# Kernel tuning notes

Measured on AMD Instinct MI355X. Metric: run time of the kernel, lower is better.

Reference implementation:

```python
import jax, jax.numpy as jnp
import numpy as np

EPS = 1e-7  # keras.backend.epsilon()
ROUTINGS = 3
NUM_CAPSULE = 32
DIM_CAPSULE = 64


def squash(x, axis=-1):
    # NOTE: faithful to the repo's (non-standard) squash: x / sqrt(||x||^2 + eps)
    s = jnp.sum(jnp.square(x), axis=axis, keepdims=True)
    return x / jnp.sqrt(s + EPS)


def setup_inputs() -> dict:
    key = jax.random.key(0)
    k1, k2 = jax.random.split(key)
    B, N_in, D_in = 64, 1024, 512
    u_vecs = jax.random.normal(k1, (B, N_in, D_in), dtype=jnp.float32)
    # shared capsule kernel: (1, input_dim, num_capsule * dim_capsule)
    W = jax.random.normal(k2, (1, D_in, NUM_CAPSULE * DIM_CAPSULE), dtype=jnp.float32) * (1.0 / np.sqrt(D_in))
    return {"u_vecs": u_vecs, "W": W}


def reference(u_vecs, W):
    B, N_in, D_in = u_vecs.shape
    # K.conv1d with a width-1 kernel == pointwise matmul
    u_hat = jnp.einsum('bid,dz->biz', u_vecs, W[0])  # [B, N_in, NC*DC]
    u_hat = u_hat.reshape(B, N_in, NUM_CAPSULE, DIM_CAPSULE)
    u_hat = jnp.transpose(u_hat, (0, 2, 1, 3))  # [B, NC, N_in, DC]

    b = jnp.zeros((B, NUM_CAPSULE, N_in), dtype=u_hat.dtype)
    outputs = None
    for i in range(ROUTINGS):
        # original permutes b to [B, N_in, NC] and softmaxes the last axis,
        # i.e. softmax over the output-capsule axis (axis=1 here)
        c = jax.nn.softmax(b, axis=1)  # [B, NC, N_in]
        outputs = squash(jnp.einsum('bni,bnid->bnd', c, u_hat))  # [B, NC, DC]
        if i < ROUTINGS - 1:
            b = jnp.einsum('bnd,bnid->bni', outputs, u_hat)  # agreement logits
    return outputs
```

## Files before the change

kernel.cpp:

```cpp
#include <hip/hip_runtime.h>

#define B_SZ   64
#define N_IN   1024
#define D_IN   512
#define NC     32
#define DC     64

typedef unsigned short u16;
typedef unsigned int   u32;
typedef __bf16 bf16x8 __attribute__((ext_vector_type(8)));
typedef _Float16 f16x8 __attribute__((ext_vector_type(8)));
typedef unsigned short u16x8 __attribute__((ext_vector_type(8)));
typedef float f32x4  __attribute__((ext_vector_type(4)));
typedef float f32x16 __attribute__((ext_vector_type(16)));

__device__ __forceinline__ float bf2f(u16 u) {
    unsigned x = ((unsigned)u) << 16;
    return __builtin_bit_cast(float, x);
}
__device__ __forceinline__ u16 f2bf(float f) {
    unsigned x = __builtin_bit_cast(unsigned, f);
    unsigned r = (x + 0x7fffu + ((x >> 16) & 1u)) >> 16;
    return (u16)r;
}
__device__ __forceinline__ u16 f2h(float f) {
    return __builtin_bit_cast(u16, (_Float16)f);
}
__device__ __forceinline__ float h2f(u16 h) {
    return (float)__builtin_bit_cast(_Float16, h);
}

#define ASYNC_LDS16(g, l) __builtin_amdgcn_global_load_lds( \
    (const __attribute__((address_space(1))) void*)(g),     \
    (__attribute__((address_space(3))) void*)(l), 16, 0, 0)

__global__ __launch_bounds__(256) void conv_all(const float* __restrict__ A,
                                                const float* __restrict__ W,
                                                u16* __restrict__ Ab,
                                                u16* __restrict__ Wb,
                                                float* __restrict__ Arowp) {
    const int tid = threadIdx.x;
    if (blockIdx.x >= 1024) {
        const int wb = blockIdx.x - 1024;
#pragma unroll
        for (int it = 0; it < 16; ++it) {
            int i = wb * 4096 + it * 256 + tid;
            float4 v = ((const float4*)W)[i];
            uint2 pk;
            pk.x = (u32)f2bf(v.x) | ((u32)f2bf(v.y) << 16);
            pk.y = (u32)f2bf(v.z) | ((u32)f2bf(v.w) << 16);
            ((uint2*)Wb)[i] = pk;
        }
        return;
    }
    const int b  = blockIdx.x >> 4;
    const int r0 = (blockIdx.x & 15) << 6;
    const int q  = tid & 127;
    const int rh = tid >> 7;
    const size_t rowbase = (size_t)(b * N_IN + r0);
    float a0 = 0.f, a1 = 0.f, a2 = 0.f, a3 = 0.f;
    for (int r = rh; r < 64; r += 2) {
        float4 v = *(const float4*)(A + (rowbase + r) * 512 + q * 4);
        a0 += v.x; a1 += v.y; a2 += v.z; a3 += v.w;
        uint2 pk;
        pk.x = (u32)f2bf(v.x) | ((u32)f2bf(v.y) << 16);
        pk.y = (u32)f2bf(v.z) | ((u32)f2bf(v.w) << 16);
        *(uint2*)(Ab + (rowbase + r) * 512 + q * 4) = pk;
    }
    const int slot = (blockIdx.x & 15) * 2 + rh;
    float* ar = Arowp + ((size_t)b * 32 + slot) * 512 + q * 4;
    ar[0] = a0; ar[1] = a1; ar[2] = a2; ar[3] = a3;
}

__global__ __launch_bounds__(256) void s0_squash(const float* __restrict__ Arowp,
                                                 const u16* __restrict__ Wb,
                                                 float* __restrict__ outs) {
    __shared__ float Al[2 * 512];
    const int tid = threadIdx.x;
    const int z   = blockIdx.x * 256 + tid;
    const int bg  = blockIdx.y * 2;

    for (int t = tid; t < 1024; t += 256) {
        int bb = t >> 9, k = t & 511;
        const float* p = Arowp + ((size_t)(bg + bb) * 32) * 512 + k;
        float s = 0.f;
#pragma unroll
        for (int j = 0; j < 32; ++j) s += p[(size_t)j * 512];
        Al[t] = s;
    }
    __syncthreads();

    float acc[2] = {};
    for (int k = 0; k < 512; ++k) {
        float wv = bf2f(Wb[(size_t)k * 2048 + z]);
        acc[0] += Al[k] * wv;
        acc[1] += Al[512 + k] * wv;
    }
#pragma unroll
    for (int bb = 0; bb < 2; ++bb) {
        float v = acc[bb] * 0.03125f;
        float sq = v * v;
        for (int off = 32; off; off >>= 1) sq += __shfl_xor(sq, off);
        outs[(size_t)(bg + bb) * 2048 + z] = v * (1.0f / sqrtf(sq + 1e-7f));
    }
}

__global__ __launch_bounds__(256) void g_pack(const u16* __restrict__ Wb,
                                              const float* __restrict__ outs,
                                              u16* __restrict__ Gpack) {
    __shared__ float vl[64 * 132];
    const int tid = threadIdx.x;
    const int kt  = blockIdx.x;
    const int np  = blockIdx.y;

    for (int t = tid; t < 8192; t += 256) {
        int b = t >> 7, idx = t & 127;
        vl[b * 132 + idx] = outs[(size_t)b * 2048 + np * 128 + idx];
    }
    __syncthreads();

    const int bs = tid & 15;
    const int k  = kt * 16 + (tid >> 4);
    float acc[4][2] = {};
#pragma unroll
    for (int n2 = 0; n2 < 2; ++n2) {
        const u16* wr = Wb + (size_t)k * 2048 + (np * 2 + n2) * 64;
#pragma unroll
        for (int d8 = 0; d8 < 8; ++d8) {
            u16x8 w8 = *(const u16x8*)&wr[d8 * 8];
            float wf[8];
#pragma unroll
            for (int j = 0; j < 8; ++j) wf[j] = bf2f(w8[j]);
#pragma unroll
            for (int bb = 0; bb < 4; ++bb) {
                const float* vp = &vl[(bs + 16 * bb) * 132 + n2 * 64 + d8 * 8];
                f32x4 va = *(const f32x4*)vp;
                f32x4 vb = *(const f32x4*)(vp + 4);
#pragma unroll
                for (int j = 0; j < 4; ++j) {
                    acc[bb][n2] += wf[j]     * va[j];
                    acc[bb][n2] += wf[j + 4] * vb[j];
                }
            }
        }
    }
    const int kk = k >> 5, kq = k & 31;
#pragma unroll
    for (int bb = 0; bb < 4; ++bb)
#pragma unroll
        for (int n2 = 0; n2 < 2; ++n2) {
            int b = bs + 16 * bb, n = np * 2 + n2;
            Gpack[(((size_t)b * 16 + kk) * 32 + n) * 32 + kq] = f2bf(acc[bb][n2]);
        }
}

__global__ __launch_bounds__(256, 2) void routing_mfma(const u16* __restrict__ Ab,
                                                       const u16* __restrict__ Gpack,
                                                       u16* __restrict__ Mp) {
    __shared__ u16 Al[64 * 512];
    __shared__ u16 clb[64 * 34];
    const int tid   = threadIdx.x;
    const int lane  = tid & 63;
    const int w     = __builtin_amdgcn_readfirstlane(tid >> 6);
    const int b     = blockIdx.x >> 4;
    const int chunk = blockIdx.x & 15;
    const int row0  = chunk * 64;

    const size_t rowbase = (size_t)(b * N_IN + row0);
#pragma unroll
    for (int rr = 0; rr < 16; ++rr) {
        const int r   = w * 16 + rr;
        const int sig = (lane & 56) | ((lane & 7) ^ (r & 7));
        ASYNC_LDS16(Ab + (rowbase + r) * 512 + sig * 8, &Al[r * 512]);
    }
    __syncthreads();

    const int quad = lane >> 4;
    const int l16  = lane & 15;
    f32x4 lacc[2] = {};
    const u16* gb = Gpack + (size_t)b * 16384;
    {
        const int r  = w * 16 + l16;
        const u16* ar = &Al[r * 512];
        for (int kk = 0; kk < 16; ++kk) {
            const int c  = kk * 4 + quad;
            const int cs = (c & 56) | ((c & 7) ^ (r & 7));
            bf16x8 af = *(const bf16x8*)&ar[cs * 8];
#pragma unroll
            for (int nt = 0; nt < 2; ++nt) {
                bf16x8 bf = *(const bf16x8*)&gb[(kk * 32 + nt * 16 + l16) * 32 + quad * 8];
                lacc[nt] = __builtin_amdgcn_mfma_f32_16x16x32_bf16(af, bf, lacc[nt], 0, 0, 0);
            }
        }
    }

#pragma unroll
    for (int reg = 0; reg < 4; ++reg) {
        float m = fmaxf(lacc[0][reg], lacc[1][reg]);
        m = fmaxf(m, __shfl_xor(m, 1));
        m = fmaxf(m, __shfl_xor(m, 2));
        m = fmaxf(m, __shfl_xor(m, 4));
        m = fmaxf(m, __shfl_xor(m, 8));
        float e0 = __expf(lacc[0][reg] - m);
        float e1 = __expf(lacc[1][reg] - m);
        float s = e0 + e1;
        s += __shfl_xor(s, 1);
        s += __shfl_xor(s, 2);
        s += __shfl_xor(s, 4);
        s += __shfl_xor(s, 8);
        float inv = 1.f / s;
        const int row = w * 16 + quad * 4 + reg;
        clb[row * 34 + l16]      = f2bf(e0 * inv);
        clb[row * 34 + 16 + l16] = f2bf(e1 * inv);
    }
    __syncthreads();

    const int h   = lane >> 5;
    const int l32 = lane & 31;
    bf16x8 cfrag[4];
#pragma unroll
    for (int kk2 = 0; kk2 < 4; ++kk2) {
        u16x8 t;
#pragma unroll
        for (int j = 0; j < 8; ++j)
            t[j] = clb[(kk2 * 16 + h * 8 + j) * 34 + l32];
        cfrag[kk2] = __builtin_bit_cast(bf16x8, t);
    }
    u16* mpb = Mp + ((size_t)b * 16 + chunk) * 32 * 512;
    for (int cti = 0; cti < 4; ++cti) {
        const int ct   = w * 4 + cti;
        const int kcol = ct * 32 + l32;
        const int c2   = kcol >> 3;
        const int e    = kcol & 7;
        f32x16 acc = {};
#pragma unroll
        for (int kk2 = 0; kk2 < 4; ++kk2) {
            u16x8 t;
#pragma unroll
            for (int j = 0; j < 8; ++j) {
                const int r2  = kk2 * 16 + h * 8 + j;
                const int cs2 = (c2 & 56) | ((c2 & 7) ^ (r2 & 7));
                t[j] = Al[r2 * 512 + cs2 * 8 + e];
            }
            bf16x8 bf = __builtin_bit_cast(bf16x8, t);
            acc = __builtin_amdgcn_mfma_f32_32x32x16_bf16(cfrag[kk2], bf, acc, 0, 0, 0);
        }
#pragma unroll
        for (int reg = 0; reg < 16; ++reg) {
            const int n = (reg & 3) + 8 * (reg >> 2) + 4 * h;
            mpb[(size_t)n * 512 + kcol] = f2h(acc[reg]);
        }
    }
}

__global__ __launch_bounds__(256, 1) void s_final_mfma(const u16* __restrict__ Mp,
                                                       const u16* __restrict__ Wb,
                                                       float* __restrict__ outs,
                                                       float* __restrict__ outf) {
    __shared__ __align__(16) u16 Wf[32768];
    __shared__ __align__(16) u16 Mlh[16 * 512];
    __shared__ float Sout[8][64];
    const int tid = threadIdx.x;
    const int n   = blockIdx.x;
    const int bg  = blockIdx.y * 8;

    for (int t = tid; t < 8192; t += 256) {
        int k = t >> 4, d4 = t & 15;
        uint2 raw = *(const uint2*)(Wb + (size_t)k * 2048 + n * 64 + d4 * 4);
        u16 bfv[4] = { (u16)(raw.x & 0xffffu), (u16)(raw.x >> 16),
                       (u16)(raw.y & 0xffffu), (u16)(raw.y >> 16) };
        const int kk = k >> 5, quad = (k >> 3) & 3, j = k & 7;
#pragma unroll
        for (int m = 0; m < 4; ++m) {
            int d = d4 * 4 + m, dtile = d >> 4, col = d & 15;
            Wf[(((dtile * 16 + kk) * 4 + quad) * 16 + col) * 8 + j] = f2h(bf2f(bfv[m]));
        }
    }
    for (int t = tid; t < 2048; t += 256) {
        int bs = t >> 8, kp = t & 255;
        const u32* p = (const u32*)(Mp + (((size_t)(bg + bs) * 16) * 32 + n) * 512) + kp;
        float s0 = 0.f, s1 = 0.f;
#pragma unroll
        for (int ch = 0; ch < 16; ++ch) {
            u32 v = p[(size_t)ch * 32 * 256];
            s0 += h2f((u16)(v & 0xffffu));
            s1 += h2f((u16)(v >> 16));
        }
        u32 pk = (u32)f2h(s0) | ((u32)f2h(s1) << 16);
        ((u32*)Mlh)[(bs * 256 + kp) ^ ((bs & 7) << 2)] = pk;
    }
    for (int t = tid; t < 2048; t += 256) ((u32*)Mlh)[2048 + t] = 0;
    __syncthreads();

    const int lane = tid & 63;
    const int w    = tid >> 6;
    const int quad = lane >> 4, l16 = lane & 15;
    f32x4 acc = {};
    for (int kk = 0; kk < 16; ++kk) {
        const int abyte = (l16 * 1024 + kk * 64 + quad * 16) ^ ((l16 & 7) << 4);
        u16x8 a = *(const u16x8*)((const char*)Mlh + abyte);
        u16x8 bfr = *(const u16x8*)&Wf[(((w * 16 + kk) * 4 + quad) * 16 + l16) * 8];
        acc = __builtin_amdgcn_mfma_f32_16x16x32_f16(__builtin_bit_cast(f16x8, a),
                                                     __builtin_bit_cast(f16x8, bfr),
                                                     acc, 0, 0, 0);
    }
    if (quad < 2) {
#pragma unroll
        for (int reg = 0; reg < 4; ++reg)
            Sout[quad * 4 + reg][w * 16 + l16] = acc[reg];
    }
    __syncthreads();

    const int w2 = tid >> 6, d = tid & 63;
#pragma unroll
    for (int i = 0; i < 2; ++i) {
        const int row = w2 * 2 + i, b = bg + row;
        float v = Sout[row][d];
        float sq = v * v;
        for (int off = 32; off; off >>= 1) sq += __shfl_xor(sq, off);
        float o = v * (1.0f / sqrtf(sq + 1e-7f));
        size_t idx = (size_t)b * 2048 + n * 64 + d;
        outs[idx] = o;
        if (outf) outf[idx] = o;
    }
}

extern "C" void kernel_launch(void* const* d_in, const int* in_sizes, int n_in,
                              void* d_out, int out_size, void* d_ws, size_t ws_size,
                              hipStream_t stream) {
    (void)in_sizes; (void)n_in; (void)out_size; (void)ws_size;
    const float* A = (const float*)d_in[0];
    const float* W = (const float*)d_in[1];
    float* out     = (float*)d_out;

    uint8_t* ws = (uint8_t*)d_ws;
    const size_t AB_B    = (size_t)B_SZ * N_IN * D_IN * 2;
    const size_t AROWP_B = (size_t)B_SZ * 32 * D_IN * 4;
    const size_t OUTS_B  = (size_t)B_SZ * NC * DC * 4;
    const size_t GP_B    = (size_t)B_SZ * 16 * 32 * 32 * 2;
    const size_t WB_B    = (size_t)D_IN * NC * DC * 2;
    u16*   Ab    = (u16*)ws;
    float* Arowp = (float*)(ws + AB_B);
    float* outs  = (float*)(ws + AB_B + AROWP_B);
    u16*   Gpack = (u16*)(ws + AB_B + AROWP_B + OUTS_B);
    u16*   Wb    = (u16*)(ws + AB_B + AROWP_B + OUTS_B + GP_B);
    u16*   Mp    = (u16*)(ws + AB_B + AROWP_B + OUTS_B + GP_B + WB_B);

    conv_all<<<1088, 256, 0, stream>>>(A, W, Ab, Wb, Arowp);

    s0_squash<<<dim3(8, 32), 256, 0, stream>>>(Arowp, Wb, outs);

    for (int it = 0; it < 2; ++it) {
        g_pack<<<dim3(32, 16), 256, 0, stream>>>(Wb, outs, Gpack);
        routing_mfma<<<1024, 256, 0, stream>>>(Ab, Gpack, Mp);
        s_final_mfma<<<dim3(32, 8), 256, 0, stream>>>(Mp, Wb, outs, it == 1 ? out : nullptr);
    }
}
```

Baseline: 361.2 us.

## Process four row chunks per routing block with double-buffered async loads

The routing kernel now runs 256 blocks, each covering four 64-row chunks of a batch instead of one, with the next chunk's A tile prefetched asynchronously into a second LDS buffer while the current one is processed. Partial M sums accumulate in registers across chunks, so only 4 partials per batch go to global memory instead of 16, and the final kernel reduces over 4 instead of 16. The cost is doubled LDS (64KB+) and occupancy dropping to one block per CU, with only 256 blocks on a 256-CU part, which may leave latency less hidden.

```diff
diff --git a/kernel.cpp b/kernel.cpp
--- a/kernel.cpp
+++ b/kernel.cpp
@@ -154,106 +154,128 @@
         }
 }
 
-__global__ __launch_bounds__(256, 2) void routing_mfma(const u16* __restrict__ Ab,
+__global__ __launch_bounds__(256, 1) void routing_mfma(const u16* __restrict__ Ab,
                                                        const u16* __restrict__ Gpack,
-                                                       u16* __restrict__ Mp) {
-    __shared__ u16 Al[64 * 512];
+                                                       u16* __restrict__ Mlp) {
+    __shared__ u16 Al[2][64 * 512];
     __shared__ u16 clb[64 * 34];
     const int tid   = threadIdx.x;
     const int lane  = tid & 63;
     const int w     = __builtin_amdgcn_readfirstlane(tid >> 6);
-    const int b     = blockIdx.x >> 4;
-    const int chunk = blockIdx.x & 15;
-    const int row0  = chunk * 64;
-
-    const size_t rowbase = (size_t)(b * N_IN + row0);
+    const int b     = blockIdx.x >> 2;
+    const int g     = blockIdx.x & 3;
+
+    const int quad = lane >> 4;
+    const int l16  = lane & 15;
+    const int h    = lane >> 5;
+    const int l32  = lane & 31;
+    const u16* gb = Gpack + (size_t)b * 16384;
+    const size_t bbase = (size_t)b * N_IN;
+
 #pragma unroll
     for (int rr = 0; rr < 16; ++rr) {
         const int r   = w * 16 + rr;
         const int sig = (lane & 56) | ((lane & 7) ^ (r & 7));
-        ASYNC_LDS16(Ab + (rowbase + r) * 512 + sig * 8, &Al[r * 512]);
-    }
-    __syncthreads();
-
-    const int quad = lane >> 4;
-    const int l16  = lane & 15;
-    f32x4 lacc[2] = {};
-    const u16* gb = Gpack + (size_t)b * 16384;
-    {
-        const int r  = w * 16 + l16;
-        const u16* ar = &Al[r * 512];
-        for (int kk = 0; kk < 16; ++kk) {
-            const int c  = kk * 4 + quad;
-            const int cs = (c & 56) | ((c & 7) ^ (r & 7));
-            bf16x8 af = *(const bf16x8*)&ar[cs * 8];
-#pragma unroll
-            for (int nt = 0; nt < 2; ++nt) {
-                bf16x8 bf = *(const bf16x8*)&gb[(kk * 32 + nt * 16 + l16) * 32 + quad * 8];
-                lacc[nt] = __builtin_amdgcn_mfma_f32_16x16x32_bf16(af, bf, lacc[nt], 0, 0, 0);
+        ASYNC_LDS16(Ab + (bbase + (size_t)(g * 4) * 64 + r) * 512 + sig * 8,
+                    &Al[0][r * 512]);
+    }
+
+    f32x16 acc4[4] = {};
+
+    for (int cc = 0; cc < 4; ++cc) {
+        const int buf = cc & 1;
+        __syncthreads();
+
+        if (cc < 3) {
+#pragma unroll
+            for (int rr = 0; rr < 16; ++rr) {
+                const int r   = w * 16 + rr;
+                const int sig = (lane & 56) | ((lane & 7) ^ (r & 7));
+                ASYNC_LDS16(Ab + (bbase + (size_t)(g * 4 + cc + 1) * 64 + r) * 512 + sig * 8,
+                            &Al[buf ^ 1][r * 512]);
             }
         }
-    }
-
-#pragma unroll
-    for (int reg = 0; reg < 4; ++reg) {
-        float m = fmaxf(lacc[0][reg], lacc[1][reg]);
-        m = fmaxf(m, __shfl_xor(m, 1));
-        m = fmaxf(m, __shfl_xor(m, 2));
-        m = fmaxf(m, __shfl_xor(m, 4));
-        m = fmaxf(m, __shfl_xor(m, 8));
-        float e0 = __expf(lacc[0][reg] - m);
-        float e1 = __expf(lacc[1][reg] - m);
-        float s = e0 + e1;
-        s += __shfl_xor(s, 1);
-        s += __shfl_xor(s, 2);
-        s += __shfl_xor(s, 4);
-        s += __shfl_xor(s, 8);
-        float inv = 1.f / s;
-        const int row = w * 16 + quad * 4 + reg;
-        clb[row * 34 + l16]      = f2bf(e0 * inv);
-        clb[row * 34 + 16 + l16] = f2bf(e1 * inv);
-    }
-    __syncthreads();
-
-    const int h   = lane >> 5;
-    const int l32 = lane & 31;
-    bf16x8 cfrag[4];
-#pragma unroll
-    for (int kk2 = 0; kk2 < 4; ++kk2) {
-        u16x8 t;
-#pragma unroll
-        for (int j = 0; j < 8; ++j)
-            t[j] = clb[(kk2 * 16 + h * 8 + j) * 34 + l32];
-        cfrag[kk2] = __builtin_bit_cast(bf16x8, t);
-    }
-    u16* mpb = Mp + ((size_t)b * 16 + chunk) * 32 * 512;
-    for (int cti = 0; cti < 4; ++cti) {
-        const int ct   = w * 4 + cti;
-        const int kcol = ct * 32 + l32;
-        const int c2   = kcol >> 3;
-        const int e    = kcol & 7;
-        f32x16 acc = {};
+
+        f32x4 lacc[2] = {};
+        {
+            const int r  = w * 16 + l16;
+            const u16* ar = &Al[buf][r * 512];
+            for (int kk = 0; kk < 16; ++kk) {
+                const int c  = kk * 4 + quad;
+                const int cs = (c & 56) | ((c & 7) ^ (r & 7));
+                bf16x8 af = *(const bf16x8*)&ar[cs * 8];
+#pragma unroll
+                for (int nt = 0; nt < 2; ++nt) {
+                    bf16x8 bf = *(const bf16x8*)&gb[(kk * 32 + nt * 16 + l16) * 32 + quad * 8];
+                    lacc[nt] = __builtin_amdgcn_mfma_f32_16x16x32_bf16(af, bf, lacc[nt], 0, 0, 0);
+                }
+            }
+        }
+
+#pragma unroll
+        for (int reg = 0; reg < 4; ++reg) {
+            float m = fmaxf(lacc[0][reg], lacc[1][reg]);
+            m = fmaxf(m, __shfl_xor(m, 1));
+            m = fmaxf(m, __shfl_xor(m, 2));
+            m = fmaxf(m, __shfl_xor(m, 4));
+            m = fmaxf(m, __shfl_xor(m, 8));
+            float e0 = __expf(lacc[0][reg] - m);
+            float e1 = __expf(lacc[1][reg] - m);
+            float s = e0 + e1;
+            s += __shfl_xor(s, 1);
+            s += __shfl_xor(s, 2);
+            s += __shfl_xor(s, 4);
+            s += __shfl_xor(s, 8);
+            float inv = 1.f / s;
+            const int row = w * 16 + quad * 4 + reg;
+            clb[row * 34 + l16]      = f2bf(e0 * inv);
+            clb[row * 34 + 16 + l16] = f2bf(e1 * inv);
+        }
+        __syncthreads();
+
+        bf16x8 cfrag[4];
 #pragma unroll
         for (int kk2 = 0; kk2 < 4; ++kk2) {
             u16x8 t;
 #pragma unroll
-            for (int j = 0; j < 8; ++j) {
-                const int r2  = kk2 * 16 + h * 8 + j;
-                const int cs2 = (c2 & 56) | ((c2 & 7) ^ (r2 & 7));
-                t[j] = Al[r2 * 512 + cs2 * 8 + e];
+            for (int j = 0; j < 8; ++j)
+                t[j] = clb[(kk2 * 16 + h * 8 + j) * 34 + l32];
+            cfrag[kk2] = __builtin_bit_cast(bf16x8, t);
+        }
+#pragma unroll
+        for (int cti = 0; cti < 4; ++cti) {
+            const int ct   = w * 4 + cti;
+            const int kcol = ct * 32 + l32;
+            const int c2   = kcol >> 3;
+            const int e    = kcol & 7;
+#pragma unroll
+            for (int kk2 = 0; kk2 < 4; ++kk2) {
+                u16x8 t;
+#pragma unroll
+                for (int j = 0; j < 8; ++j) {
+                    const int r2  = kk2 * 16 + h * 8 + j;
+                    const int cs2 = (c2 & 56) | ((c2 & 7) ^ (r2 & 7));
+                    t[j] = Al[buf][r2 * 512 + cs2 * 8 + e];
+                }
+                bf16x8 bf = __builtin_bit_cast(bf16x8, t);
+                acc4[cti] = __builtin_amdgcn_mfma_f32_32x32x16_bf16(cfrag[kk2], bf, acc4[cti], 0, 0, 0);
             }
-            bf16x8 bf = __builtin_bit_cast(bf16x8, t);
-            acc = __builtin_amdgcn_mfma_f32_32x32x16_bf16(cfrag[kk2], bf, acc, 0, 0, 0);
-        }
+        }
+    }
+
+    u16* mpb = Mlp + (((size_t)b * 4 + g) * 32) * 512;
+#pragma unroll
+    for (int cti = 0; cti < 4; ++cti) {
+        const int kcol = (w * 4 + cti) * 32 + l32;
 #pragma unroll
         for (int reg = 0; reg < 16; ++reg) {
             const int n = (reg & 3) + 8 * (reg >> 2) + 4 * h;
-            mpb[(size_t)n * 512 + kcol] = f2h(acc[reg]);
-        }
-    }
-}
-
-__global__ __launch_bounds__(256, 1) void s_final_mfma(const u16* __restrict__ Mp,
+            mpb[(size_t)n * 512 + kcol] = f2h(acc4[cti][reg]);
+        }
+    }
+}
+
+__global__ __launch_bounds__(256, 1) void s_final_mfma(const u16* __restrict__ Mlp,
                                                        const u16* __restrict__ Wb,
                                                        float* __restrict__ outs,
                                                        float* __restrict__ outf) {
@@ -278,11 +300,11 @@
     }
     for (int t = tid; t < 2048; t += 256) {
         int bs = t >> 8, kp = t & 255;
-        const u32* p = (const u32*)(Mp + (((size_t)(bg + bs) * 16) * 32 + n) * 512) + kp;
+        const u32* p = (const u32*)Mlp + (((size_t)(bg + bs) * 4) * 32 + n) * 256 + kp;
         float s0 = 0.f, s1 = 0.f;
 #pragma unroll
-        for (int ch = 0; ch < 16; ++ch) {
-            u32 v = p[(size_t)ch * 32 * 256];
+        for (int gg = 0; gg < 4; ++gg) {
+            u32 v = p[(size_t)gg * 32 * 256];
             s0 += h2f((u16)(v & 0xffffu));
             s1 += h2f((u16)(v >> 16));
         }
@@ -344,7 +366,7 @@
     float* outs  = (float*)(ws + AB_B + AROWP_B);
     u16*   Gpack = (u16*)(ws + AB_B + AROWP_B + OUTS_B);
     u16*   Wb    = (u16*)(ws + AB_B + AROWP_B + OUTS_B + GP_B);
-    u16*   Mp    = (u16*)(ws + AB_B + AROWP_B + OUTS_B + GP_B + WB_B);
+    u16*   Mlp   = (u16*)(ws + AB_B + AROWP_B + OUTS_B + GP_B + WB_B);
 
     conv_all<<<1088, 256, 0, stream>>>(A, W, Ab, Wb, Arowp);
 
@@ -352,7 +374,7 @@
 
     for (int it = 0; it < 2; ++it) {
         g_pack<<<dim3(32, 16), 256, 0, stream>>>(Wb, outs, Gpack);
-        routing_mfma<<<1024, 256, 0, stream>>>(Ab, Gpack, Mp);
-        s_final_mfma<<<dim3(32, 8), 256, 0, stream>>>(Mp, Wb, outs, it == 1 ? out : nullptr);
-    }
-}
+        routing_mfma<<<256, 256, 0, stream>>>(Ab, Gpack, Mlp);
+        s_final_mfma<<<dim3(32, 8), 256, 0, stream>>>(Mlp, Wb, outs, it == 1 ? out : nullptr);
+    }
+}
```

Measured after the change: 353.3 us. 2.2% less time.
